# Optimization experiments

Measured on AMD Instinct MI355X. Metric: run time of the kernel, lower is better.

## Reference

```python
import jax, jax.numpy as jnp
import numpy as np

N_NODES = 50000
N_EDGES = 800000
IN_DIM = 89
HID = 128


def gcn_conv(x, src, dst, deg_inv_sqrt, W, b):
    # PyG GCNConv: x' = D^{-1/2} (A + I) D^{-1/2} (x W) + b
    h = x @ W  # [N, F_out]
    norm = deg_inv_sqrt[src] * deg_inv_sqrt[dst]  # per-edge norm [E]
    msgs = h[src] * norm[:, None]  # gather + scale [E, F_out]
    agg = jax.ops.segment_sum(msgs, dst, num_segments=x.shape[0])
    # self-loop contribution: norm = deg_inv_sqrt[i]^2
    agg = agg + h * (deg_inv_sqrt * deg_inv_sqrt)[:, None]
    return agg + b


def setup_inputs() -> dict:
    key = jax.random.key(0)
    k1, k2, k3, k4, k5, k6 = jax.random.split(key, 6)
    x = jax.random.normal(k1, (N_NODES, IN_DIM), dtype=jnp.float32)
    edge_index = jax.random.randint(k2, (2, N_EDGES), 0, N_NODES, dtype=jnp.int64)
    # Glorot-style init for GCN weights
    W1 = jax.random.normal(k3, (IN_DIM, HID), dtype=jnp.float32) * (1.0 / np.sqrt(IN_DIM))
    b1 = jnp.zeros((HID,), dtype=jnp.float32)
    W2 = jax.random.normal(k4, (HID, HID), dtype=jnp.float32) * (1.0 / np.sqrt(HID))
    b2 = jnp.zeros((HID,), dtype=jnp.float32)
    return {"x": x, "edge_index": edge_index, "W1": W1, "b1": b1, "W2": W2, "b2": b2}


def reference(x, edge_index, W1, b1, W2, b2):
    src = edge_index[0]
    dst = edge_index[1]
    n = x.shape[0]
    # degree of A + I: 1 (self loop) + in-degree
    deg = 1.0 + jax.ops.segment_sum(jnp.ones((src.shape[0],), x.dtype), dst, num_segments=n)
    deg_inv_sqrt = jax.lax.rsqrt(deg)
    h = jax.nn.relu(gcn_conv(x, src, dst, deg_inv_sqrt, W1, b1))
    h = jax.nn.relu(gcn_conv(h, src, dst, deg_inv_sqrt, W2, b2))
    return (h, edge_index)
```

## Files before the change

kernel.cpp:

```cpp
#include <hip/hip_runtime.h>
#include <hip/hip_bf16.h>


#define HID 128
#define KIN 89
#define KP 128
#define BSH 7
#define BNODES 128
#define MAXBUCK 512
#define NPB 128
#define P4CAP 3072

typedef __attribute__((ext_vector_type(8))) short bf16x8;
typedef __attribute__((ext_vector_type(4))) float f32x4;

static __device__ inline float2 unpack_bf16(unsigned v) {
    union { unsigned u; float f; } lo, hi;
    lo.u = v << 16;
    hi.u = v & 0xFFFF0000u;
    return make_float2(lo.f, hi.f);
}

static __device__ inline unsigned pack_bf16(float a, float b) {
    __hip_bfloat162 h = __float22bfloat162_rn(make_float2(a, b));
    return *reinterpret_cast<unsigned*>(&h);
}

static __device__ inline unsigned short f2bf(float v) {
    __hip_bfloat16 h = __float2bfloat16(v);
    return *reinterpret_cast<unsigned short*>(&h);
}

__global__ __launch_bounds__(256) void p1_kernel(
    const int* __restrict__ ei, float* __restrict__ outE,
    int* __restrict__ histG,
    const float* __restrict__ W1, unsigned short* __restrict__ W1t,
    const float* __restrict__ W2, unsigned short* __restrict__ W2t,
    int E, int nbuck)
{
    __shared__ int h[MAXBUCK];
    const int tid = threadIdx.x, blk = blockIdx.x;
    const int* src = ei;
    const int* dst = ei + E;
    for (int b = tid; b < nbuck; b += 256) h[b] = 0;

    int tg = blk * 256 + tid;
    if (tg < HID * KP) {
        int n = tg / KP, k = tg % KP;
        W1t[tg] = f2bf(k < KIN ? W1[(size_t)k * HID + n] : 0.0f);
    } else {
        int t2 = tg - HID * KP;
        if (t2 < HID * HID) {
            int n = t2 / HID, k = t2 % HID;
            W2t[t2] = f2bf(W2[(size_t)k * HID + n]);
        }
    }
    __syncthreads();

    const int chunk = (E + NPB - 1) / NPB;
    const int beg = blk * chunk, end = min(beg + chunk, E);
    for (int i = beg + tid; i < end; i += 256) {
        int d = dst[i];
        atomicAdd(&h[d >> BSH], 1);
        outE[i] = (float)src[i];
        outE[E + i] = (float)d;
    }
    __syncthreads();
    for (int b = tid; b < nbuck; b += 256) histG[b * NPB + blk] = h[b];
}

__global__ __launch_bounds__(NPB) void p2a_kernel(
    int* __restrict__ histG, int* __restrict__ totals)
{
    __shared__ int wsum[NPB / 64];
    const int b = blockIdx.x, tid = threadIdx.x, lane = tid & 63, wid = tid >> 6;
    int c = histG[b * NPB + tid];
    int s = c;
#pragma unroll
    for (int off = 1; off < 64; off <<= 1) {
        int t = __shfl_up(s, off, 64);
        if (lane >= off) s += t;
    }
    if (lane == 63) wsum[wid] = s;
    __syncthreads();
    if (tid == 0) {
        int a = 0;
#pragma unroll
        for (int w = 0; w < NPB / 64; ++w) { int t = wsum[w]; wsum[w] = a; a += t; }
    }
    __syncthreads();
    int excl = wsum[wid] + s - c;
    histG[b * NPB + tid] = excl;
    if (tid == NPB - 1) totals[b] = excl + c;
}

static __device__ inline void scan_totals2(const int* __restrict__ totals,
                                           int* __restrict__ sexcl,
                                           int* __restrict__ wsum,
                                           int nbuck, int tid)
{
    const int lane = tid & 63, wid = tid >> 6;
    const int i0 = 2 * tid, i1 = 2 * tid + 1;
    int t0 = (i0 < nbuck) ? totals[i0] : 0;
    int t1 = (i1 < nbuck) ? totals[i1] : 0;
    int p = t0 + t1;
    int s = p;
#pragma unroll
    for (int off = 1; off < 64; off <<= 1) {
        int t = __shfl_up(s, off, 64);
        if (lane >= off) s += t;
    }
    if (lane == 63) wsum[wid] = s;
    __syncthreads();
    if (tid == 0) {
        int a = 0;
#pragma unroll
        for (int w = 0; w < 4; ++w) { int t = wsum[w]; wsum[w] = a; a += t; }
    }
    __syncthreads();
    int excl = wsum[wid] + s - p;
    sexcl[i0] = excl;
    sexcl[i1] = excl + t0;
}

__global__ __launch_bounds__(256) void p3_part_kernel(
    const int* __restrict__ ei, const int* __restrict__ histG,
    const int* __restrict__ totals, unsigned* __restrict__ ebuf,
    int E, int nbuck)
{
    __shared__ int cur[MAXBUCK];
    __shared__ int wsum[4];
    const int tid = threadIdx.x, blk = blockIdx.x;
    const int* src = ei;
    const int* dst = ei + E;
    scan_totals2(totals, cur, wsum, nbuck, tid);
    __syncthreads();
    for (int b = tid; b < nbuck; b += 256) cur[b] += histG[b * NPB + blk];
    const int chunk = (E + NPB - 1) / NPB;
    const int beg = blk * chunk, end = min(beg + chunk, E);
    __syncthreads();
    for (int i = beg + tid; i < end; i += 256) {
        int d = dst[i];
        int b = d >> BSH;
        int pos = atomicAdd(&cur[b], 1);
        ebuf[pos] = ((unsigned)(d & (BNODES - 1)) << 16) | (unsigned)src[i];
    }
}

__global__ __launch_bounds__(256) void p4_sort_kernel(
    const unsigned* __restrict__ ebuf, const int* __restrict__ totals,
    unsigned short* __restrict__ csr, int* __restrict__ rowptr,
    float* __restrict__ dis, int N, int E, int nbuck)
{
    __shared__ int counts[BNODES];
    __shared__ int cursor[BNODES];
    __shared__ int sbase[MAXBUCK];
    __shared__ int wsum[4];
    __shared__ int w2[2];
    __shared__ unsigned short staging[P4CAP];
    const int b = blockIdx.x, tid = threadIdx.x, lane = tid & 63, wid = tid >> 6;

    scan_totals2(totals, sbase, wsum, nbuck, tid);
    __syncthreads();
    const int gbase = sbase[b];
    const int cnt = totals[b];

    if (tid < BNODES) counts[tid] = 0;
    __syncthreads();
    for (int i = tid; i < cnt; i += 256)
        atomicAdd(&counts[ebuf[gbase + i] >> 16], 1);
    __syncthreads();

    int c = 0, s = 0;
    if (tid < BNODES) {
        c = counts[tid];
        s = c;
#pragma unroll
        for (int off = 1; off < 64; off <<= 1) {
            int t = __shfl_up(s, off, 64);
            if (lane >= off) s += t;
        }
        if (lane == 63) w2[wid] = s;
    }
    __syncthreads();
    if (tid == 0) { int t = w2[0]; w2[0] = 0; w2[1] = t; }
    __syncthreads();
    if (tid < BNODES) {
        int excl = w2[wid] + s - c;
        cursor[tid] = excl;
        int node = b * BNODES + tid;
        if (node < N) {
            rowptr[node] = gbase + excl;
            dis[node] = rsqrtf(1.0f + (float)c);
        }
    }
    if (b == 0 && tid == 0) rowptr[N] = E;
    __syncthreads();

    if (cnt <= P4CAP) {
        for (int i = tid; i < cnt; i += 256) {
            unsigned v = ebuf[gbase + i];
            int pos = atomicAdd(&cursor[v >> 16], 1);
            staging[pos] = (unsigned short)(v & 0xFFFFu);
        }
        __syncthreads();
        for (int i = tid; i < cnt; i += 256)
            csr[gbase + i] = staging[i];
    } else {
        for (int i = tid; i < cnt; i += 256) {
            unsigned v = ebuf[gbase + i];
            int pos = atomicAdd(&cursor[v >> 16], 1);
            csr[gbase + pos] = (unsigned short)(v & 0xFFFFu);
        }
    }
}

__global__ __launch_bounds__(256) void xconv_kernel(
    const float* __restrict__ X, const float* __restrict__ dis,
    unsigned* __restrict__ Xhs, int N)
{
    int t = blockIdx.x * 256 + threadIdx.x;
    if (t >= N * (KP / 2)) return;
    int n = t / (KP / 2), c = t % (KP / 2);
    float d = dis[n];
    const float* xr = X + (size_t)n * KIN;
    float a = (2 * c     < KIN) ? d * xr[2 * c]     : 0.0f;
    float b = (2 * c + 1 < KIN) ? d * xr[2 * c + 1] : 0.0f;
    Xhs[t] = pack_bf16(a, b);
}

__global__ __launch_bounds__(256) void gather_kernel(
    const uint2* __restrict__ rows, const int* __restrict__ rowptr,
    const unsigned short* __restrict__ csr, uint2* __restrict__ aggh, int N)
{
    int node = blockIdx.x * 4 + (threadIdx.x >> 6);
    if (node >= N) return;
    const int lane = threadIdx.x & 63;
    const int half = lane >> 5;
    const int sl   = lane & 31;

    float a0 = 0.0f, a1 = 0.0f, a2 = 0.0f, a3 = 0.0f;
    if (half == 0) {
        uint2 sv = rows[(size_t)node * 32 + sl];
        float2 lo = unpack_bf16(sv.x), hi = unpack_bf16(sv.y);
        a0 = lo.x; a1 = lo.y; a2 = hi.x; a3 = hi.y;
    }

    const int beg = rowptr[node], end = rowptr[node + 1];
    int j = beg;
    for (; j + 8 <= end; j += 8) {
        int r0 = csr[j     + half];
        int r1 = csr[j + 2 + half];
        int r2 = csr[j + 4 + half];
        int r3 = csr[j + 6 + half];
        uint2 v0 = rows[(size_t)r0 * 32 + sl];
        uint2 v1 = rows[(size_t)r1 * 32 + sl];
        uint2 v2 = rows[(size_t)r2 * 32 + sl];
        uint2 v3 = rows[(size_t)r3 * 32 + sl];
        float2 p;
        p = unpack_bf16(v0.x); a0 += p.x; a1 += p.y;
        p = unpack_bf16(v0.y); a2 += p.x; a3 += p.y;
        p = unpack_bf16(v1.x); a0 += p.x; a1 += p.y;
        p = unpack_bf16(v1.y); a2 += p.x; a3 += p.y;
        p = unpack_bf16(v2.x); a0 += p.x; a1 += p.y;
        p = unpack_bf16(v2.y); a2 += p.x; a3 += p.y;
        p = unpack_bf16(v3.x); a0 += p.x; a1 += p.y;
        p = unpack_bf16(v3.y); a2 += p.x; a3 += p.y;
    }
    for (; j + 4 <= end; j += 4) {
        int r0 = csr[j     + half];
        int r1 = csr[j + 2 + half];
        uint2 v0 = rows[(size_t)r0 * 32 + sl];
        uint2 v1 = rows[(size_t)r1 * 32 + sl];
        float2 p;
        p = unpack_bf16(v0.x); a0 += p.x; a1 += p.y;
        p = unpack_bf16(v0.y); a2 += p.x; a3 += p.y;
        p = unpack_bf16(v1.x); a0 += p.x; a1 += p.y;
        p = unpack_bf16(v1.y); a2 += p.x; a3 += p.y;
    }
    for (; j < end; j += 2) {
        int idx = j + half;
        if (idx < end) {
            int r = csr[idx];
            uint2 v = rows[(size_t)r * 32 + sl];
            float2 lo = unpack_bf16(v.x), hi = unpack_bf16(v.y);
            a0 += lo.x; a1 += lo.y; a2 += hi.x; a3 += hi.y;
        }
    }

    a0 += __shfl_xor(a0, 32, 64);
    a1 += __shfl_xor(a1, 32, 64);
    a2 += __shfl_xor(a2, 32, 64);
    a3 += __shfl_xor(a3, 32, 64);
    if (half == 0)
        aggh[(size_t)node * 32 + sl] =
            make_uint2(pack_bf16(a0, a1), pack_bf16(a2, a3));
}

template<int KPA, bool LAYER1>
__global__ __launch_bounds__(256) void mfma_gemm_kernel(
    const unsigned short* __restrict__ A, const unsigned short* __restrict__ Wt,
    const float* __restrict__ bias, const float* __restrict__ dis,
    void* __restrict__ outp, int N)
{
    const int wave = threadIdx.x >> 6;
    const int lane = threadIdx.x & 63;
    const int m    = lane & 15;
    const int quad = lane >> 4;
    const int row0 = blockIdx.x * 64 + wave * 16;
    const int node = row0 + m;

    f32x4 acc[8];
#pragma unroll
    for (int t = 0; t < 8; ++t) acc[t] = (f32x4){0.0f, 0.0f, 0.0f, 0.0f};

    const int arow = min(node, N - 1);
    const unsigned short* arp = A + (size_t)arow * KPA;

#pragma unroll
    for (int c = 0; c < KPA / 32; ++c) {
        const int k0 = c * 32 + quad * 8;
        bf16x8 nv = *(const bf16x8*)(arp + k0);
#pragma unroll
        for (int t = 0; t < 8; ++t) {
            bf16x8 wv = *(const bf16x8*)(Wt + (size_t)(t * 16 + m) * KPA + k0);
            acc[t] = __builtin_amdgcn_mfma_f32_16x16x32_bf16(wv, nv, acc[t], 0, 0, 0);
        }
    }

    if (node < N) {
        const float dv = dis[node];
#pragma unroll
        for (int t = 0; t < 8; ++t) {
            const int col0 = t * 16 + quad * 4;
            float4 bb = *(const float4*)&bias[col0];
            float r0 = fmaxf(fmaf(dv, acc[t][0], bb.x), 0.0f);
            float r1 = fmaxf(fmaf(dv, acc[t][1], bb.y), 0.0f);
            float r2 = fmaxf(fmaf(dv, acc[t][2], bb.z), 0.0f);
            float r3 = fmaxf(fmaf(dv, acc[t][3], bb.w), 0.0f);
            if (LAYER1) {
                uint2 u;
                u.x = pack_bf16(r0 * dv, r1 * dv);
                u.y = pack_bf16(r2 * dv, r3 * dv);
                *(uint2*)((unsigned short*)outp + (size_t)node * HID + col0) = u;
            } else {
                float4 r = make_float4(r0, r1, r2, r3);
                *(float4*)((float*)outp + (size_t)node * HID + col0) = r;
            }
        }
    }
}


static inline char* wsal(char*& p, size_t n) {
    uintptr_t q = ((uintptr_t)p + 255) & ~(uintptr_t)255;
    char* r = (char*)q;
    p = r + n;
    return r;
}

extern "C" void kernel_launch(void* const* d_in, const int* in_sizes, int n_in,
                              void* d_out, int out_size, void* d_ws, size_t ws_size,
                              hipStream_t stream) {
    const float* x  = (const float*)d_in[0];
    const int*   ei = (const int*)d_in[1];
    const float* W1 = (const float*)d_in[2];
    const float* b1 = (const float*)d_in[3];
    const float* W2 = (const float*)d_in[4];
    const float* b2 = (const float*)d_in[5];

    const int N = in_sizes[0] / KIN;
    const int E = in_sizes[1] / 2;
    const int nbuck = (N + BNODES - 1) >> BSH;

    float* out  = (float*)d_out;
    float* outH = out;
    float* outE = out + (size_t)N * HID;

    char* ws = (char*)d_ws;
    int*            histG  = (int*)wsal(ws, (size_t)MAXBUCK * NPB * 4);
    int*            totals = (int*)wsal(ws, MAXBUCK * 4);
    int*            rowptr = (int*)wsal(ws, (size_t)(N + 1) * 4);
    float*          dis    = (float*)wsal(ws, (size_t)N * 4);
    unsigned*       ebuf   = (unsigned*)wsal(ws, (size_t)E * 4);
    unsigned short* csr    = (unsigned short*)wsal(ws, (size_t)E * 2);
    unsigned*       Xhs    = (unsigned*)wsal(ws, (size_t)N * (KP / 2) * 4);
    unsigned*       agg1h  = (unsigned*)wsal(ws, (size_t)N * (KP / 2) * 4);
    unsigned short* g2h    = (unsigned short*)wsal(ws, (size_t)N * HID * 2);
    unsigned short* agg2h  = (unsigned short*)wsal(ws, (size_t)N * HID * 2);
    unsigned short* W1t    = (unsigned short*)wsal(ws, (size_t)HID * KP * 2);
    unsigned short* W2t    = (unsigned short*)wsal(ws, (size_t)HID * HID * 2);

    p1_kernel<<<NPB, 256, 0, stream>>>(ei, outE, histG, W1, W1t, W2, W2t, E, nbuck);
    p2a_kernel<<<nbuck, NPB, 0, stream>>>(histG, totals);
    p3_part_kernel<<<NPB, 256, 0, stream>>>(ei, histG, totals, ebuf, E, nbuck);
    p4_sort_kernel<<<nbuck, 256, 0, stream>>>(ebuf, totals, csr, rowptr, dis,
                                              N, E, nbuck);
    xconv_kernel<<<(N * (KP / 2) + 255) / 256, 256, 0, stream>>>(x, dis, Xhs, N);

    const int ngt = (N + 3) / 4;
    const int ngm = (N + 63) / 64;

    gather_kernel<<<ngt, 256, 0, stream>>>((const uint2*)Xhs, rowptr, csr,
                                           (uint2*)agg1h, N);
    mfma_gemm_kernel<KP, true><<<ngm, 256, 0, stream>>>(
        (const unsigned short*)agg1h, W1t, b1, dis, g2h, N);

    gather_kernel<<<ngt, 256, 0, stream>>>((const uint2*)g2h, rowptr, csr,
                                           (uint2*)agg2h, N);
    mfma_gemm_kernel<HID, false><<<ngm, 256, 0, stream>>>(
        agg2h, W2t, b2, dis, outH, N);
}
```

Before: 232.3 us.

## Fuse preprocessing kernels into one cooperative kernel with grid syncs

Merges the histogram, scan, partition, per-bucket sort and feature conversion kernels into a single cooperative launch with nbuck blocks, using grid.sync between phases in place of separate kernel launches. The edge partition is now split across nbuck (about 391) blocks rather than 128, and the per-bucket histogram scan is done row-wise across blocks. The aim is to remove launch gaps and inter-kernel drain; in exchange it adds grid-wide barrier cost and requires all blocks to be co-resident.

```diff
diff --git a/kernel.cpp b/kernel.cpp
--- a/kernel.cpp
+++ b/kernel.cpp
@@ -1,5 +1,8 @@
 #include <hip/hip_runtime.h>
 #include <hip/hip_bf16.h>
+#include <hip/hip_cooperative_groups.h>
+
+namespace cg = cooperative_groups;
 
 
 #define HID 128
@@ -8,7 +11,6 @@
 #define BSH 7
 #define BNODES 128
 #define MAXBUCK 512
-#define NPB 128
 #define P4CAP 3072
 
 typedef __attribute__((ext_vector_type(8))) short bf16x8;
@@ -29,69 +31,6 @@
 static __device__ inline unsigned short f2bf(float v) {
     __hip_bfloat16 h = __float2bfloat16(v);
     return *reinterpret_cast<unsigned short*>(&h);
-}
-
-__global__ __launch_bounds__(256) void p1_kernel(
-    const int* __restrict__ ei, float* __restrict__ outE,
-    int* __restrict__ histG,
-    const float* __restrict__ W1, unsigned short* __restrict__ W1t,
-    const float* __restrict__ W2, unsigned short* __restrict__ W2t,
-    int E, int nbuck)
-{
-    __shared__ int h[MAXBUCK];
-    const int tid = threadIdx.x, blk = blockIdx.x;
-    const int* src = ei;
-    const int* dst = ei + E;
-    for (int b = tid; b < nbuck; b += 256) h[b] = 0;
-
-    int tg = blk * 256 + tid;
-    if (tg < HID * KP) {
-        int n = tg / KP, k = tg % KP;
-        W1t[tg] = f2bf(k < KIN ? W1[(size_t)k * HID + n] : 0.0f);
-    } else {
-        int t2 = tg - HID * KP;
-        if (t2 < HID * HID) {
-            int n = t2 / HID, k = t2 % HID;
-            W2t[t2] = f2bf(W2[(size_t)k * HID + n]);
-        }
-    }
-    __syncthreads();
-
-    const int chunk = (E + NPB - 1) / NPB;
-    const int beg = blk * chunk, end = min(beg + chunk, E);
-    for (int i = beg + tid; i < end; i += 256) {
-        int d = dst[i];
-        atomicAdd(&h[d >> BSH], 1);
-        outE[i] = (float)src[i];
-        outE[E + i] = (float)d;
-    }
-    __syncthreads();
-    for (int b = tid; b < nbuck; b += 256) histG[b * NPB + blk] = h[b];
-}
-
-__global__ __launch_bounds__(NPB) void p2a_kernel(
-    int* __restrict__ histG, int* __restrict__ totals)
-{
-    __shared__ int wsum[NPB / 64];
-    const int b = blockIdx.x, tid = threadIdx.x, lane = tid & 63, wid = tid >> 6;
-    int c = histG[b * NPB + tid];
-    int s = c;
-#pragma unroll
-    for (int off = 1; off < 64; off <<= 1) {
-        int t = __shfl_up(s, off, 64);
-        if (lane >= off) s += t;
-    }
-    if (lane == 63) wsum[wid] = s;
-    __syncthreads();
-    if (tid == 0) {
-        int a = 0;
-#pragma unroll
-        for (int w = 0; w < NPB / 64; ++w) { int t = wsum[w]; wsum[w] = a; a += t; }
-    }
-    __syncthreads();
-    int excl = wsum[wid] + s - c;
-    histG[b * NPB + tid] = excl;
-    if (tid == NPB - 1) totals[b] = excl + c;
 }
 
 static __device__ inline void scan_totals2(const int* __restrict__ totals,
@@ -123,47 +62,104 @@
     sexcl[i1] = excl + t0;
 }
 
-__global__ __launch_bounds__(256) void p3_part_kernel(
-    const int* __restrict__ ei, const int* __restrict__ histG,
-    const int* __restrict__ totals, unsigned* __restrict__ ebuf,
-    int E, int nbuck)
+__global__ __launch_bounds__(256) void preproc_kernel(
+    const int* __restrict__ ei, float* __restrict__ outE,
+    const float* __restrict__ X,
+    const float* __restrict__ W1, unsigned short* __restrict__ W1t,
+    const float* __restrict__ W2, unsigned short* __restrict__ W2t,
+    int* __restrict__ histG, int* __restrict__ totals,
+    int* __restrict__ rowptr, float* __restrict__ dis,
+    unsigned* __restrict__ ebuf, unsigned short* __restrict__ csr,
+    unsigned* __restrict__ Xhs,
+    int N, int E, int nbuck)
 {
-    __shared__ int cur[MAXBUCK];
+    __shared__ int sA[MAXBUCK];
     __shared__ int wsum[4];
+    __shared__ int counts[BNODES];
+    __shared__ int cursor[BNODES];
+    __shared__ int w2[2];
+    __shared__ unsigned short staging[P4CAP];
+
+    cg::grid_group grid = cg::this_grid();
     const int tid = threadIdx.x, blk = blockIdx.x;
+    const int npart = gridDim.x;
     const int* src = ei;
     const int* dst = ei + E;
-    scan_totals2(totals, cur, wsum, nbuck, tid);
-    __syncthreads();
-    for (int b = tid; b < nbuck; b += 256) cur[b] += histG[b * NPB + blk];
-    const int chunk = (E + NPB - 1) / NPB;
+    const int chunk = (E + npart - 1) / npart;
     const int beg = blk * chunk, end = min(beg + chunk, E);
+    const int lane = tid & 63, wid = tid >> 6;
+
+    for (int b = tid; b < nbuck; b += 256) sA[b] = 0;
+
+    int tg = blk * 256 + tid;
+    if (tg < HID * KP) {
+        int n = tg / KP, k = tg % KP;
+        W1t[tg] = f2bf(k < KIN ? W1[(size_t)k * HID + n] : 0.0f);
+    } else {
+        int t2 = tg - HID * KP;
+        if (t2 < HID * HID) {
+            int n = t2 / HID, k = t2 % HID;
+            W2t[t2] = f2bf(W2[(size_t)k * HID + n]);
+        }
+    }
+    __syncthreads();
+
+    for (int i = beg + tid; i < end; i += 256) {
+        int d = dst[i];
+        atomicAdd(&sA[d >> BSH], 1);
+        outE[i] = (float)src[i];
+        outE[E + i] = (float)d;
+    }
+    __syncthreads();
+    for (int b = tid; b < nbuck; b += 256) histG[(size_t)b * MAXBUCK + blk] = sA[b];
+
+    grid.sync();
+
+    {
+        int* row = histG + (size_t)blk * MAXBUCK;
+        const int i0 = 2 * tid, i1 = i0 + 1;
+        int t0 = (i0 < npart) ? row[i0] : 0;
+        int t1 = (i1 < npart) ? row[i1] : 0;
+        int p = t0 + t1;
+        int s = p;
+#pragma unroll
+        for (int off = 1; off < 64; off <<= 1) {
+            int t = __shfl_up(s, off, 64);
+            if (lane >= off) s += t;
+        }
+        if (lane == 63) wsum[wid] = s;
+        __syncthreads();
+        if (tid == 0) {
+            int a = 0;
+#pragma unroll
+            for (int w = 0; w < 4; ++w) { int t = wsum[w]; wsum[w] = a; a += t; }
+            totals[blk] = a;
+        }
+        __syncthreads();
+        int excl = wsum[wid] + s - p;
+        if (i0 < npart) row[i0] = excl;
+        if (i1 < npart) row[i1] = excl + t0;
+    }
+
+    grid.sync();
+
+    scan_totals2(totals, sA, wsum, nbuck, tid);
+    __syncthreads();
+    for (int b = tid; b < nbuck; b += 256) sA[b] += histG[(size_t)b * MAXBUCK + blk];
     __syncthreads();
     for (int i = beg + tid; i < end; i += 256) {
         int d = dst[i];
         int b = d >> BSH;
-        int pos = atomicAdd(&cur[b], 1);
+        int pos = atomicAdd(&sA[b], 1);
         ebuf[pos] = ((unsigned)(d & (BNODES - 1)) << 16) | (unsigned)src[i];
     }
-}
-
-__global__ __launch_bounds__(256) void p4_sort_kernel(
-    const unsigned* __restrict__ ebuf, const int* __restrict__ totals,
-    unsigned short* __restrict__ csr, int* __restrict__ rowptr,
-    float* __restrict__ dis, int N, int E, int nbuck)
-{
-    __shared__ int counts[BNODES];
-    __shared__ int cursor[BNODES];
-    __shared__ int sbase[MAXBUCK];
-    __shared__ int wsum[4];
-    __shared__ int w2[2];
-    __shared__ unsigned short staging[P4CAP];
-    const int b = blockIdx.x, tid = threadIdx.x, lane = tid & 63, wid = tid >> 6;
-
-    scan_totals2(totals, sbase, wsum, nbuck, tid);
-    __syncthreads();
-    const int gbase = sbase[b];
-    const int cnt = totals[b];
+
+    grid.sync();
+
+    scan_totals2(totals, sA, wsum, nbuck, tid);
+    __syncthreads();
+    const int gbase = sA[blk];
+    const int cnt = totals[blk];
 
     if (tid < BNODES) counts[tid] = 0;
     __syncthreads();
@@ -188,13 +184,13 @@
     if (tid < BNODES) {
         int excl = w2[wid] + s - c;
         cursor[tid] = excl;
-        int node = b * BNODES + tid;
+        int node = blk * BNODES + tid;
         if (node < N) {
             rowptr[node] = gbase + excl;
             dis[node] = rsqrtf(1.0f + (float)c);
         }
     }
-    if (b == 0 && tid == 0) rowptr[N] = E;
+    if (blk == 0 && tid == 0) rowptr[N] = E;
     __syncthreads();
 
     if (cnt <= P4CAP) {
@@ -213,20 +209,18 @@
             csr[gbase + pos] = (unsigned short)(v & 0xFFFFu);
         }
     }
-}
-
-__global__ __launch_bounds__(256) void xconv_kernel(
-    const float* __restrict__ X, const float* __restrict__ dis,
-    unsigned* __restrict__ Xhs, int N)
-{
-    int t = blockIdx.x * 256 + threadIdx.x;
-    if (t >= N * (KP / 2)) return;
-    int n = t / (KP / 2), c = t % (KP / 2);
-    float d = dis[n];
-    const float* xr = X + (size_t)n * KIN;
-    float a = (2 * c     < KIN) ? d * xr[2 * c]     : 0.0f;
-    float b = (2 * c + 1 < KIN) ? d * xr[2 * c + 1] : 0.0f;
-    Xhs[t] = pack_bf16(a, b);
+
+    grid.sync();
+
+    const int totalw = N * (KP / 2);
+    for (int t = blk * 256 + tid; t < totalw; t += npart * 256) {
+        int n = t / (KP / 2), cc = t % (KP / 2);
+        float d = dis[n];
+        const float* xr = X + (size_t)n * KIN;
+        float a = (2 * cc     < KIN) ? d * xr[2 * cc]     : 0.0f;
+        float b = (2 * cc + 1 < KIN) ? d * xr[2 * cc + 1] : 0.0f;
+        Xhs[t] = pack_bf16(a, b);
+    }
 }
 
 __global__ __launch_bounds__(256) void gather_kernel(
@@ -369,16 +363,16 @@
     const float* W2 = (const float*)d_in[4];
     const float* b2 = (const float*)d_in[5];
 
-    const int N = in_sizes[0] / KIN;
-    const int E = in_sizes[1] / 2;
-    const int nbuck = (N + BNODES - 1) >> BSH;
+    int N = in_sizes[0] / KIN;
+    int E = in_sizes[1] / 2;
+    int nbuck = (N + BNODES - 1) >> BSH;
 
     float* out  = (float*)d_out;
     float* outH = out;
     float* outE = out + (size_t)N * HID;
 
     char* ws = (char*)d_ws;
-    int*            histG  = (int*)wsal(ws, (size_t)MAXBUCK * NPB * 4);
+    int*            histG  = (int*)wsal(ws, (size_t)MAXBUCK * MAXBUCK * 4);
     int*            totals = (int*)wsal(ws, MAXBUCK * 4);
     int*            rowptr = (int*)wsal(ws, (size_t)(N + 1) * 4);
     float*          dis    = (float*)wsal(ws, (size_t)N * 4);
@@ -391,12 +385,17 @@
     unsigned short* W1t    = (unsigned short*)wsal(ws, (size_t)HID * KP * 2);
     unsigned short* W2t    = (unsigned short*)wsal(ws, (size_t)HID * HID * 2);
 
-    p1_kernel<<<NPB, 256, 0, stream>>>(ei, outE, histG, W1, W1t, W2, W2t, E, nbuck);
-    p2a_kernel<<<nbuck, NPB, 0, stream>>>(histG, totals);
-    p3_part_kernel<<<NPB, 256, 0, stream>>>(ei, histG, totals, ebuf, E, nbuck);
-    p4_sort_kernel<<<nbuck, 256, 0, stream>>>(ebuf, totals, csr, rowptr, dis,
-                                              N, E, nbuck);
-    xconv_kernel<<<(N * (KP / 2) + 255) / 256, 256, 0, stream>>>(x, dis, Xhs, N);
+    {
+        void* args[] = {
+            (void*)&ei, (void*)&outE, (void*)&x,
+            (void*)&W1, (void*)&W1t, (void*)&W2, (void*)&W2t,
+            (void*)&histG, (void*)&totals, (void*)&rowptr, (void*)&dis,
+            (void*)&ebuf, (void*)&csr, (void*)&Xhs,
+            (void*)&N, (void*)&E, (void*)&nbuck
+        };
+        hipLaunchCooperativeKernel((const void*)preproc_kernel,
+                                   dim3(nbuck), dim3(256), args, 0, stream);
+    }
 
     const int ngt = (N + 3) / 4;
     const int ngm = (N + 63) / 64;
```

Result: slower. 445.0 us (+91.6%).
